# Optimization experiments

Hardware: AMD Instinct MI355X
Metric: run time of the kernel (lower is better)

## Reference

```python
import jax, jax.numpy as jnp
import numpy as np

N, Q, D = 8, 900, 256
HB, WB = 200, 200
L, NH, P = 6, 8, 4
HD = D // NH
FF = 512
NCLS, NBOX = 10, 8
ODIM = NCLS + NBOX
THRESH = 0.5
OFFSET_SCALE = 1.0
SCALE = 1.0 / float(np.sqrt(HD))


def _ln(x, g, b, eps=1e-5):
    m = jnp.mean(x, axis=-1, keepdims=True)
    v = jnp.mean((x - m) ** 2, axis=-1, keepdims=True)
    return (x - m) * jax.lax.rsqrt(v + eps) * g + b


def _mha(x, Wq, bq, Wk, bk, Wv, bv, Wo, bo):
    q = (x @ Wq + bq).reshape(N, Q, NH, HD)
    k = (x @ Wk + bk).reshape(N, Q, NH, HD)
    v = (x @ Wv + bv).reshape(N, Q, NH, HD)
    att = jax.nn.softmax(jnp.einsum('bqhd,bkhd->bhqk', q, k) * SCALE, axis=-1)
    o = jnp.einsum('bhqk,bkhd->bqhd', att, v).reshape(N, Q, D)
    return o @ Wo + bo


def _deform(q, ref, bev, dv_W, dv_b, off_W, off_b, aw_W, aw_b, do_W, do_b):
    # value projection of BEV map: (N, HW, D) -> (N, NH, HW, HD)
    val = (bev @ dv_W + dv_b).reshape(N, HB * WB, NH, HD).transpose(0, 2, 1, 3)
    off = (q @ off_W + off_b).reshape(N, Q, NH, P, 2)
    aw = jax.nn.softmax((q @ aw_W + aw_b).reshape(N, Q, NH, P), axis=-1)
    # ref: (N,Q,1,2) pixel coords -> broadcast to (N,Q,NH,P,2)
    loc = ref[:, :, :, None, :] + off * OFFSET_SCALE
    x = jnp.clip(loc[..., 0], 0.0, WB - 1.0)
    y = jnp.clip(loc[..., 1], 0.0, HB - 1.0)
    x0 = jnp.floor(x)
    y0 = jnp.floor(y)
    x1 = jnp.minimum(x0 + 1.0, WB - 1.0)
    y1 = jnp.minimum(y0 + 1.0, HB - 1.0)
    wx = (x - x0).transpose(0, 2, 1, 3)[..., None]  # (N,NH,Q,P,1)
    wy = (y - y0).transpose(0, 2, 1, 3)[..., None]

    def gather(ix, iy):
        idx = (iy * WB + ix).astype(jnp.int32)               # (N,Q,NH,P)
        idx = idx.transpose(0, 2, 1, 3).reshape(N, NH, Q * P, 1)
        g = jnp.take_along_axis(val, idx, axis=2)            # (N,NH,Q*P,HD)
        return g.reshape(N, NH, Q, P, HD)

    samp = (gather(x0, y0) * (1 - wx) * (1 - wy)
            + gather(x1, y0) * wx * (1 - wy)
            + gather(x0, y1) * (1 - wx) * wy
            + gather(x1, y1) * wx * wy)                      # (N,NH,Q,P,HD)
    awt = aw.transpose(0, 2, 1, 3)                           # (N,NH,Q,P)
    out = jnp.einsum('bhqp,bhqpd->bqhd', awt, samp).reshape(N, Q, D)
    return out @ do_W + do_b


def _ref_points():
    # n_sample=Q points evenly spread over the HBxWB grid, pixel coords, unnormalized
    idx = jnp.round(jnp.linspace(0.0, HB * WB - 1.0, Q)).astype(jnp.int32)
    x = (idx % WB).astype(jnp.float32)
    y = (idx // WB).astype(jnp.float32)
    rp = jnp.stack([x, y], axis=-1)                          # (Q,2)
    return jnp.broadcast_to(rp[None, :, None, :], (N, Q, 1, 2))


def _det(x, W1, b1, W2, b2):
    h = jax.nn.relu(x @ W1 + b1)
    o = h @ W2 + b2
    return jnp.concatenate([jax.nn.sigmoid(o[..., :NCLS]), o[..., NCLS:]], axis=-1)


def setup_inputs() -> dict:
    key = jax.random.key(0)
    ks = iter(jax.random.split(key, 48))

    def w(shape, s=0.02):
        return jax.random.normal(next(ks), shape, jnp.float32) * s

    inp = {
        'bev_features': jax.random.normal(next(ks), (N, HB * WB, D), jnp.float32),
        'pos_emb': w((Q, D), 1.0),
        'Wq': w((L, D, D)), 'bq': jnp.zeros((L, D), jnp.float32),
        'Wk': w((L, D, D)), 'bk': jnp.zeros((L, D), jnp.float32),
        'Wv': w((L, D, D)), 'bv': jnp.zeros((L, D), jnp.float32),
        'Wo': w((L, D, D)), 'bo': jnp.zeros((L, D), jnp.float32),
        'ln1_g': jnp.ones((L, D), jnp.float32), 'ln1_b': jnp.zeros((L, D), jnp.float32),
        'ln2_g': jnp.ones((L, D), jnp.float32), 'ln2_b': jnp.zeros((L, D), jnp.float32),
        'ln3_g': jnp.ones((L, D), jnp.float32), 'ln3_b': jnp.zeros((L, D), jnp.float32),
        'dv_W': w((L, D, D)), 'dv_b': jnp.zeros((L, D), jnp.float32),
        'off_W': w((L, D, NH * P * 2), 0.01), 'off_b': jnp.zeros((L, NH * P * 2), jnp.float32),
        'aw_W': w((L, D, NH * P), 0.01), 'aw_b': jnp.zeros((L, NH * P), jnp.float32),
        'do_W': w((L, D, D)), 'do_b': jnp.zeros((L, D), jnp.float32),
        'f1_W': w((L, D, FF)), 'f1_b': jnp.zeros((L, FF), jnp.float32),
        'f2_W': w((L, FF, D)), 'f2_b': jnp.zeros((L, D), jnp.float32),
        'det_W1': w((D, D)), 'det_b1': jnp.zeros((D,), jnp.float32),
        'det_W2': w((D, ODIM)), 'det_b2': jnp.zeros((ODIM,), jnp.float32),
    }
    return inp


def reference(bev_features, pos_emb, Wq, bq, Wk, bk, Wv, bv, Wo, bo,
              ln1_g, ln1_b, ln2_g, ln2_b, ln3_g, ln3_b,
              dv_W, dv_b, off_W, off_b, aw_W, aw_b, do_W, do_b,
              f1_W, f1_b, f2_W, f2_b, det_W1, det_b1, det_W2, det_b2):
    queries = jnp.broadcast_to(pos_emb[None], (N, Q, D))
    ref = _ref_points()
    output = queries
    layer_results = []
    for i in range(L):
        x = output + queries
        a = _mha(x, Wq[i], bq[i], Wk[i], bk[i], Wv[i], bv[i], Wo[i], bo[i])
        x2 = _ln(x + a, ln1_g[i], ln1_b[i])
        d = _deform(x2, ref, bev_features, dv_W[i], dv_b[i], off_W[i], off_b[i],
                    aw_W[i], aw_b[i], do_W[i], do_b[i])
        x3 = _ln(x2 + d, ln2_g[i], ln2_b[i])
        f = jax.nn.relu(x3 @ f1_W[i] + f1_b[i]) @ f2_W[i] + f2_b[i]
        output = _ln(x3 + f, ln3_g[i], ln3_b[i])
        layer_results.append(_det(output, det_W1, det_b1, det_W2, det_b2))
    layer_results = jnp.stack(layer_results, axis=0)   # (L,N,Q,ODIM)
    detections = layer_results[-1]
    track_mask = detections[..., 0] >= THRESH
    return output, detections, track_mask, layer_results
```

## Files before the change

### kernel.cpp

```cpp
#include <hip/hip_runtime.h>
#include <hip/hip_bf16.h>
#include <math.h>

#define N 8
#define Q 900
#define D 256
#define HB 200
#define WB 200
#define L 6
#define NH 8
#define P 4
#define HD 32
#define FF 512
#define NCLS 10
#define ODIM 18
#define HW (HB*WB)
#define NQ (N*Q)
#define NQD (NQ*D)
#define QD (Q*D)
#define SCALE 0.17677669529663687f

typedef __attribute__((ext_vector_type(4))) float f32x4;
typedef __attribute__((ext_vector_type(8))) short short8v;

__device__ __forceinline__ short bf16_of(float f) {
  __hip_bfloat16 h = __float2bfloat16(f);
  return __builtin_bit_cast(short, h);
}

#define TM 64
#define TN 64
#define KC 128

template <int ACT>
__global__ __launch_bounds__(256) void gemm_kernel(
    const float* __restrict__ A, const float* __restrict__ B,
    const float* __restrict__ bias, float* __restrict__ C,
    int M, int K, int Nc) {
  __shared__ float AsT[KC][TM + 4];
  __shared__ float Bs[KC][TN + 4];
  const int tid = threadIdx.x;
  const int tx = tid & 15, ty = tid >> 4;
  const int m0 = blockIdx.x * TM, n0 = blockIdx.y * TN;

  float c[4][4] = {};

  for (int kc = 0; kc < K; kc += KC) {
    {
      int r = tid >> 2;
      int gr = m0 + r;
      int kb = (tid & 3) * 32;
#pragma unroll
      for (int q = 0; q < 8; ++q) {
        int k = kb + q * 4;
        float4 av = make_float4(0.f, 0.f, 0.f, 0.f);
        if (gr < M) av = *(const float4*)(A + (size_t)gr * K + kc + k);
        AsT[k + 0][r] = av.x; AsT[k + 1][r] = av.y;
        AsT[k + 2][r] = av.z; AsT[k + 3][r] = av.w;
      }
    }
    {
#pragma unroll
      for (int i = 0; i < 8; ++i) {
        int idx = i * 256 + tid;
        int kr = idx >> 4;
        int c4 = (idx & 15) * 4;
        *(float4*)&Bs[kr][c4] = *(const float4*)(B + (size_t)(kc + kr) * Nc + n0 + c4);
      }
    }
    __syncthreads();
#pragma unroll 8
    for (int kk = 0; kk < KC; ++kk) {
      float4 av = *(const float4*)&AsT[kk][ty * 4];
      float4 bv = *(const float4*)&Bs[kk][tx * 4];
      c[0][0] += av.x * bv.x; c[0][1] += av.x * bv.y; c[0][2] += av.x * bv.z; c[0][3] += av.x * bv.w;
      c[1][0] += av.y * bv.x; c[1][1] += av.y * bv.y; c[1][2] += av.y * bv.z; c[1][3] += av.y * bv.w;
      c[2][0] += av.z * bv.x; c[2][1] += av.z * bv.y; c[2][2] += av.z * bv.z; c[2][3] += av.z * bv.w;
      c[3][0] += av.w * bv.x; c[3][1] += av.w * bv.y; c[3][2] += av.w * bv.z; c[3][3] += av.w * bv.w;
    }
    __syncthreads();
  }

#pragma unroll
  for (int i = 0; i < 4; ++i) {
    int row = m0 + ty * 4 + i;
    if (row >= M) continue;
#pragma unroll
    for (int j = 0; j < 4; ++j) {
      int col = n0 + tx * 4 + j;
      float v = c[i][j] + bias[col];
      if (ACT == 1) v = fmaxf(v, 0.f);
      C[(size_t)row * Nc + col] = v;
    }
  }
}

#define TMT 64
#define TKT 16
template <int ACT>
__global__ __launch_bounds__(256) void gemm_thin_kernel(
    const float* __restrict__ A, const float* __restrict__ B,
    const float* __restrict__ bias, float* __restrict__ C,
    int M, int K, int Nc) {
  __shared__ float AsT[TKT][TMT + 4];
  __shared__ float Bs[TKT][16 + 2];
  const int tid = threadIdx.x;
  const int tx = tid & 15, ty = tid >> 4;
  const int m0 = blockIdx.x * TMT, n0 = blockIdx.y * 16;

  float c[4] = {};

  for (int kt = 0; kt < K; kt += TKT) {
    {
      int r = tid >> 2;
      int cb = (tid & 3) * 4;
      int gr = m0 + r;
      float4 av = make_float4(0.f, 0.f, 0.f, 0.f);
      if (gr < M) av = *(const float4*)(A + (size_t)gr * K + kt + cb);
      AsT[cb + 0][r] = av.x;
      AsT[cb + 1][r] = av.y;
      AsT[cb + 2][r] = av.z;
      AsT[cb + 3][r] = av.w;
    }
    {
      int r = tid >> 4;
      int cc = tid & 15;
      int gc = n0 + cc;
      Bs[r][cc] = (gc < Nc) ? B[(size_t)(kt + r) * Nc + gc] : 0.f;
    }
    __syncthreads();
#pragma unroll
    for (int kk = 0; kk < TKT; ++kk) {
      float4 av = *(const float4*)&AsT[kk][ty * 4];
      float bv = Bs[kk][tx];
      c[0] += av.x * bv; c[1] += av.y * bv; c[2] += av.z * bv; c[3] += av.w * bv;
    }
    __syncthreads();
  }

  int col = n0 + tx;
  if (col < Nc) {
    float bs = bias[col];
#pragma unroll
    for (int i = 0; i < 4; ++i) {
      int row = m0 + ty * 4 + i;
      if (row < M) {
        float v = c[i] + bs;
        if (ACT == 2 && col < NCLS) v = 1.f / (1.f + expf(-v));
        C[(size_t)row * Nc + col] = v;
      }
    }
  }
}

__global__ __launch_bounds__(256) void attn_kernel(
    const float* __restrict__ qg, const float* __restrict__ kg,
    const float* __restrict__ vg, float* __restrict__ og) {
  const int n = blockIdx.z, h = blockIdx.y;
  const int wv = threadIdx.x >> 6;
  const int lane = threadIdx.x & 63;
  const int g = lane >> 4;
  const int c = lane & 15;
  const int q0 = blockIdx.x * 64 + wv * 16;

  const float* qb = qg + (size_t)n * Q * D + h * HD;
  const float* kb = kg + (size_t)n * Q * D + h * HD;
  const float* vb = vg + (size_t)n * Q * D + h * HD;

  short8v qf = {};
  {
    int qr = q0 + c;
    if (qr < Q) {
      const float* qp = qb + (size_t)qr * D + g * 8;
#pragma unroll
      for (int j = 0; j < 8; ++j) qf[j] = bf16_of(qp[j]);
    }
  }

  const float SC2 = SCALE * 1.4426950408889634f;
  float m2 = -1e30f, l = 0.f;
  f32x4 acc0 = {0.f, 0.f, 0.f, 0.f}, acc1 = {0.f, 0.f, 0.f, 0.f};

  for (int kt0 = 0; kt0 < Q; kt0 += 64) {
    float s[16];
#pragma unroll
    for (int t = 0; t < 4; ++t) {
      short8v kf = {};
      int kr = kt0 + t * 16 + c;
      if (kr < Q) {
        const float* kp = kb + (size_t)kr * D + g * 8;
#pragma unroll
        for (int j = 0; j < 8; ++j) kf[j] = bf16_of(kp[j]);
      }
      f32x4 d = __builtin_amdgcn_mfma_f32_16x16x32_bf16(kf, qf, (f32x4){0.f, 0.f, 0.f, 0.f}, 0, 0, 0);
#pragma unroll
      for (int r = 0; r < 4; ++r) s[t * 4 + r] = d[r];
    }
#pragma unroll
    for (int t = 0; t < 4; ++t)
#pragma unroll
      for (int r = 0; r < 4; ++r) {
        int key = kt0 + t * 16 + g * 4 + r;
        s[t * 4 + r] = (key < Q) ? s[t * 4 + r] * SC2 : -1e30f;
      }
    float tm = s[0];
#pragma unroll
    for (int j = 1; j < 16; ++j) tm = fmaxf(tm, s[j]);
    tm = fmaxf(tm, __shfl_xor(tm, 16));
    tm = fmaxf(tm, __shfl_xor(tm, 32));
    float m2n = fmaxf(m2, tm);
    float corr = exp2f(m2 - m2n);
    m2 = m2n;
    float ps = 0.f;
#pragma unroll
    for (int j = 0; j < 16; ++j) { s[j] = exp2f(s[j] - m2); ps += s[j]; }
    ps += __shfl_xor(ps, 16);
    ps += __shfl_xor(ps, 32);
    l = l * corr + ps;
    float cr0 = __shfl(corr, g * 4 + 0);
    float cr1 = __shfl(corr, g * 4 + 1);
    float cr2 = __shfl(corr, g * 4 + 2);
    float cr3 = __shfl(corr, g * 4 + 3);
    acc0[0] *= cr0; acc0[1] *= cr1; acc0[2] *= cr2; acc0[3] *= cr3;
    acc1[0] *= cr0; acc1[1] *= cr1; acc1[2] *= cr2; acc1[3] *= cr3;

#pragma unroll
    for (int pr = 0; pr < 2; ++pr) {
      short8v pa, v0 = {}, v1 = {};
#pragma unroll
      for (int j = 0; j < 8; ++j) pa[j] = bf16_of(s[pr * 8 + j]);
#pragma unroll
      for (int j = 0; j < 8; ++j) {
        int key = kt0 + (pr * 2 + (j >> 2)) * 16 + g * 4 + (j & 3);
        if (key < Q) {
          const float* vp = vb + (size_t)key * D;
          v0[j] = bf16_of(vp[c]);
          v1[j] = bf16_of(vp[c + 16]);
        }
      }
      acc0 = __builtin_amdgcn_mfma_f32_16x16x32_bf16(pa, v0, acc0, 0, 0, 0);
      acc1 = __builtin_amdgcn_mfma_f32_16x16x32_bf16(pa, v1, acc1, 0, 0, 0);
    }
  }

  float inv = 1.f / l;
  float iv[4];
#pragma unroll
  for (int r = 0; r < 4; ++r) iv[r] = __shfl(inv, g * 4 + r);
#pragma unroll
  for (int r = 0; r < 4; ++r) {
    int qr = q0 + g * 4 + r;
    if (qr < Q) {
      float* op = og + (size_t)(n * Q + qr) * D + h * HD;
      op[c] = acc0[r] * iv[r];
      op[c + 16] = acc1[r] * iv[r];
    }
  }
}

__global__ __launch_bounds__(256) void ln_add_kernel(
    const float* __restrict__ A, const float* __restrict__ Bp,
    const float* __restrict__ g, const float* __restrict__ b,
    float* __restrict__ out) {
  const int wave = threadIdx.x >> 6;
  const int lane = threadIdx.x & 63;
  const int row = blockIdx.x * 4 + wave;
  const size_t base = (size_t)row * D + lane * 4;
  float4 a4 = *(const float4*)(A + base);
  float4 b4 = *(const float4*)(Bp + base);
  float v0 = a4.x + b4.x, v1 = a4.y + b4.y, v2 = a4.z + b4.z, v3 = a4.w + b4.w;
  float sum = v0 + v1 + v2 + v3;
#pragma unroll
  for (int off = 1; off < 64; off <<= 1) sum += __shfl_xor(sum, off);
  float mean = sum * (1.f / D);
  float d0 = v0 - mean, d1 = v1 - mean, d2 = v2 - mean, d3 = v3 - mean;
  float vsum = d0 * d0 + d1 * d1 + d2 * d2 + d3 * d3;
#pragma unroll
  for (int off = 1; off < 64; off <<= 1) vsum += __shfl_xor(vsum, off);
  float inv_std = 1.0f / sqrtf(vsum * (1.f / D) + 1e-5f);
  float4 g4 = *(const float4*)(g + lane * 4);
  float4 bb4 = *(const float4*)(b + lane * 4);
  float4 o4;
  o4.x = d0 * inv_std * g4.x + bb4.x;
  o4.y = d1 * inv_std * g4.y + bb4.y;
  o4.z = d2 * inv_std * g4.z + bb4.z;
  o4.w = d3 * inv_std * g4.w + bb4.w;
  *(float4*)(out + base) = o4;
}

__global__ __launch_bounds__(256) void deform_kernel(
    const float* __restrict__ bev, const float* __restrict__ offB,
    const float* __restrict__ awB, const float* __restrict__ dvW,
    const float* __restrict__ dvb, float* __restrict__ dtmp) {
  const int pb = blockIdx.x;
  const int bq0 = pb * 2;
  const int n = bq0 / Q;
  const int t = threadIdx.x;

  __shared__ float aw_s[2][NH * P];
  __shared__ int   idx_s[2][NH * P * 4];
  __shared__ float w_s[2][NH * P * 4];
  __shared__ float agg_s[2][NH][D + 4];
  __shared__ float red_s[2][4][D];

  if (t < 64) {
    int qq = t >> 5, e = t & 31;
    int bq = bq0 + qq;
    int qi = bq - n * Q;
    float tq = __fmul_rn((float)qi, 44.492767333984375f);
    int ir = (int)rintf(tq);
    float rx = (float)(ir % WB);
    float ry = (float)(ir / WB);
    float ox = offB[(size_t)bq * 64 + e * 2 + 0];
    float oy = offB[(size_t)bq * 64 + e * 2 + 1];
    float lx = fminf(fmaxf(rx + ox, 0.f), (float)(WB - 1));
    float ly = fminf(fmaxf(ry + oy, 0.f), (float)(HB - 1));
    float x0 = floorf(lx), y0 = floorf(ly);
    float x1 = fminf(x0 + 1.f, (float)(WB - 1));
    float y1 = fminf(y0 + 1.f, (float)(HB - 1));
    float wx = lx - x0, wy = ly - y0;
    int b4 = e * 4;
    idx_s[qq][b4 + 0] = (int)y0 * WB + (int)x0; w_s[qq][b4 + 0] = (1.f - wx) * (1.f - wy);
    idx_s[qq][b4 + 1] = (int)y0 * WB + (int)x1; w_s[qq][b4 + 1] = wx * (1.f - wy);
    idx_s[qq][b4 + 2] = (int)y1 * WB + (int)x0; w_s[qq][b4 + 2] = (1.f - wx) * wy;
    idx_s[qq][b4 + 3] = (int)y1 * WB + (int)x1; w_s[qq][b4 + 3] = wx * wy;
  } else if (t < 80) {
    int qq = (t - 64) >> 3, hh = (t - 64) & 7;
    const float* ap = awB + (size_t)(bq0 + qq) * 32 + hh * P;
    float l0 = ap[0], l1 = ap[1], l2 = ap[2], l3 = ap[3];
    float mx = fmaxf(fmaxf(l0, l1), fmaxf(l2, l3));
    float e0 = expf(l0 - mx), e1 = expf(l1 - mx), e2 = expf(l2 - mx), e3 = expf(l3 - mx);
    float inv = 1.f / (e0 + e1 + e2 + e3);
    aw_s[qq][hh * P + 0] = e0 * inv; aw_s[qq][hh * P + 1] = e1 * inv;
    aw_s[qq][hh * P + 2] = e2 * inv; aw_s[qq][hh * P + 3] = e3 * inv;
  }
  __syncthreads();

  {
    const float* bevn = bev + (size_t)n * HW * D;
    const int wv = t >> 6, lane = t & 63;
    const int c4 = lane * 4;
#pragma unroll
    for (int u = 0; u < 4; ++u) {
      int pid = wv + u * 4;
      int qq = pid >> 3, h = pid & 7;
      f32x4 acc = {0.f, 0.f, 0.f, 0.f};
#pragma unroll
      for (int p = 0; p < P; ++p) {
        int e = h * P + p;
        float aw = aw_s[qq][e];
        const int* ix = &idx_s[qq][e * 4];
        const float* wsp = &w_s[qq][e * 4];
        float4 g0 = *(const float4*)(bevn + (size_t)ix[0] * D + c4);
        float4 g1 = *(const float4*)(bevn + (size_t)ix[1] * D + c4);
        float4 g2 = *(const float4*)(bevn + (size_t)ix[2] * D + c4);
        float4 g3 = *(const float4*)(bevn + (size_t)ix[3] * D + c4);
        acc[0] += aw * (wsp[0] * g0.x + wsp[1] * g1.x + wsp[2] * g2.x + wsp[3] * g3.x);
        acc[1] += aw * (wsp[0] * g0.y + wsp[1] * g1.y + wsp[2] * g2.y + wsp[3] * g3.y);
        acc[2] += aw * (wsp[0] * g0.z + wsp[1] * g1.z + wsp[2] * g2.z + wsp[3] * g3.z);
        acc[3] += aw * (wsp[0] * g0.w + wsp[1] * g1.w + wsp[2] * g2.w + wsp[3] * g3.w);
      }
      *(f32x4*)&agg_s[qq][h][c4] = acc;
    }
  }
  __syncthreads();

  {
    const int chunk = t >> 6;
    const int col4 = t & 63;
    const int tt0 = col4 * 4;
    const int h = tt0 >> 5;
    f32x4 p0 = {0.f, 0.f, 0.f, 0.f}, p1 = {0.f, 0.f, 0.f, 0.f};
    const float* ag0 = agg_s[0][h];
    const float* ag1 = agg_s[1][h];
#pragma unroll 4
    for (int dd4 = 0; dd4 < 64; dd4 += 4) {
      int dd = chunk * 64 + dd4;
      float4 w0 = *(const float4*)(dvW + (size_t)(dd + 0) * D + tt0);
      float4 w1 = *(const float4*)(dvW + (size_t)(dd + 1) * D + tt0);
      float4 w2 = *(const float4*)(dvW + (size_t)(dd + 2) * D + tt0);
      float4 w3 = *(const float4*)(dvW + (size_t)(dd + 3) * D + tt0);
      float4 a0 = *(const float4*)&ag0[dd];
      float4 a1 = *(const float4*)&ag1[dd];
      p0[0] += a0.x * w0.x + a0.y * w1.x + a0.z * w2.x + a0.w * w3.x;
      p0[1] += a0.x * w0.y + a0.y * w1.y + a0.z * w2.y + a0.w * w3.y;
      p0[2] += a0.x * w0.z + a0.y * w1.z + a0.z * w2.z + a0.w * w3.z;
      p0[3] += a0.x * w0.w + a0.y * w1.w + a0.z * w2.w + a0.w * w3.w;
      p1[0] += a1.x * w0.x + a1.y * w1.x + a1.z * w2.x + a1.w * w3.x;
      p1[1] += a1.x * w0.y + a1.y * w1.y + a1.z * w2.y + a1.w * w3.y;
      p1[2] += a1.x * w0.z + a1.y * w1.z + a1.z * w2.z + a1.w * w3.z;
      p1[3] += a1.x * w0.w + a1.y * w1.w + a1.z * w2.w + a1.w * w3.w;
    }
    *(f32x4*)&red_s[0][chunk][tt0] = p0;
    *(f32x4*)&red_s[1][chunk][tt0] = p1;
  }
  __syncthreads();
  {
    float bs = dvb[t];
    dtmp[(size_t)bq0 * D + t] =
        bs + red_s[0][0][t] + red_s[0][1][t] + red_s[0][2][t] + red_s[0][3][t];
    dtmp[(size_t)(bq0 + 1) * D + t] =
        bs + red_s[1][0][t] + red_s[1][1][t] + red_s[1][2][t] + red_s[1][3][t];
  }
}

__global__ void bcast_q_kernel(const float* __restrict__ pos, float* __restrict__ out) {
  for (size_t i = (size_t)blockIdx.x * blockDim.x + threadIdx.x; i < (size_t)NQD;
       i += (size_t)gridDim.x * blockDim.x)
    out[i] = pos[i % QD];
}
__global__ void add_q_kernel(const float* __restrict__ prev, const float* __restrict__ pos,
                             float* __restrict__ x) {
  for (size_t i = (size_t)blockIdx.x * blockDim.x + threadIdx.x; i < (size_t)NQD;
       i += (size_t)gridDim.x * blockDim.x)
    x[i] = prev[i] + pos[i % QD];
}
__global__ void finalize_kernel(const float* __restrict__ lr5, float* __restrict__ det,
                                float* __restrict__ mask) {
  int i = blockIdx.x * blockDim.x + threadIdx.x;
  if (i < NQ * ODIM) det[i] = lr5[i];
  if (i < NQ) mask[i] = (lr5[(size_t)i * ODIM] >= 0.5f) ? 1.0f : 0.0f;
}

extern "C" void kernel_launch(void* const* d_in, const int* in_sizes, int n_in,
                              void* d_out, int out_size, void* d_ws, size_t ws_size,
                              hipStream_t stream) {
  const float* bev  = (const float*)d_in[0];
  const float* pos  = (const float*)d_in[1];
  const float* Wq   = (const float*)d_in[2];  const float* bq  = (const float*)d_in[3];
  const float* Wk   = (const float*)d_in[4];  const float* bk  = (const float*)d_in[5];
  const float* Wv   = (const float*)d_in[6];  const float* bv  = (const float*)d_in[7];
  const float* Wo   = (const float*)d_in[8];  const float* bo  = (const float*)d_in[9];
  const float* ln1g = (const float*)d_in[10]; const float* ln1b = (const float*)d_in[11];
  const float* ln2g = (const float*)d_in[12]; const float* ln2b = (const float*)d_in[13];
  const float* ln3g = (const float*)d_in[14]; const float* ln3b = (const float*)d_in[15];
  const float* dvW  = (const float*)d_in[16]; const float* dvb = (const float*)d_in[17];
  const float* offW = (const float*)d_in[18]; const float* offb = (const float*)d_in[19];
  const float* awW  = (const float*)d_in[20]; const float* awb = (const float*)d_in[21];
  const float* doW  = (const float*)d_in[22]; const float* dob = (const float*)d_in[23];
  const float* f1W  = (const float*)d_in[24]; const float* f1b = (const float*)d_in[25];
  const float* f2W  = (const float*)d_in[26]; const float* f2b = (const float*)d_in[27];
  const float* dW1  = (const float*)d_in[28]; const float* db1 = (const float*)d_in[29];
  const float* dW2  = (const float*)d_in[30]; const float* db2 = (const float*)d_in[31];

  float* w = (float*)d_ws;
  float* b0 = w + 0 * (size_t)NQD;
  float* b1 = w + 1 * (size_t)NQD;
  float* b2 = w + 2 * (size_t)NQD;
  float* b3 = w + 3 * (size_t)NQD;
  float* ffh = b1;
  float* offB = b0;
  float* awB  = b0 + (size_t)NQ * 64;

  float* out_output = (float*)d_out;
  float* out_det    = out_output + (size_t)NQD;
  float* out_mask   = out_det + (size_t)NQ * ODIM;
  float* out_lr     = out_mask + (size_t)NQ;

  const dim3 blk256(256);
  const dim3 gemmGridD((NQ + TM - 1) / TM, D / TN);
  const dim3 gemmGridFF((NQ + TM - 1) / TM, FF / TN);
  const dim3 thinGridOff((NQ + TMT - 1) / TMT, 4);
  const dim3 thinGridAw((NQ + TMT - 1) / TMT, 2);
  const dim3 thinGridDet((NQ + TMT - 1) / TMT, 2);
  const dim3 attnGrid((Q + 63) / 64, NH, N);
  const dim3 lnGrid(NQ / 4);
  const dim3 defGrid(NQ / 2);
  const int ewGrid = 1024;

  bcast_q_kernel<<<ewGrid, blk256, 0, stream>>>(pos, out_output);

  for (int i = 0; i < L; ++i) {
    const size_t wDD = (size_t)i * D * D;
    add_q_kernel<<<ewGrid, blk256, 0, stream>>>(out_output, pos, b0);
    gemm_kernel<0><<<gemmGridD, blk256, 0, stream>>>(b0, Wq + wDD, bq + (size_t)i * D, b1, NQ, D, D);
    gemm_kernel<0><<<gemmGridD, blk256, 0, stream>>>(b0, Wk + wDD, bk + (size_t)i * D, b2, NQ, D, D);
    gemm_kernel<0><<<gemmGridD, blk256, 0, stream>>>(b0, Wv + wDD, bv + (size_t)i * D, b3, NQ, D, D);
    attn_kernel<<<attnGrid, blk256, 0, stream>>>(b1, b2, b3, out_output);
    gemm_kernel<0><<<gemmGridD, blk256, 0, stream>>>(out_output, Wo + wDD, bo + (size_t)i * D, b1, NQ, D, D);
    ln_add_kernel<<<lnGrid, blk256, 0, stream>>>(b0, b1, ln1g + (size_t)i * D, ln1b + (size_t)i * D, b2);
    gemm_thin_kernel<0><<<thinGridOff, blk256, 0, stream>>>(b2, offW + (size_t)i * D * 64, offb + (size_t)i * 64, offB, NQ, D, 64);
    gemm_thin_kernel<0><<<thinGridAw, blk256, 0, stream>>>(b2, awW + (size_t)i * D * 32, awb + (size_t)i * 32, awB, NQ, D, 32);
    deform_kernel<<<defGrid, blk256, 0, stream>>>(bev, offB, awB, dvW + wDD, dvb + (size_t)i * D, b3);
    gemm_kernel<0><<<gemmGridD, blk256, 0, stream>>>(b3, doW + wDD, dob + (size_t)i * D, b1, NQ, D, D);
    ln_add_kernel<<<lnGrid, blk256, 0, stream>>>(b2, b1, ln2g + (size_t)i * D, ln2b + (size_t)i * D, b0);
    gemm_kernel<1><<<gemmGridFF, blk256, 0, stream>>>(b0, f1W + (size_t)i * D * FF, f1b + (size_t)i * FF, ffh, NQ, D, FF);
    gemm_kernel<0><<<gemmGridD, blk256, 0, stream>>>(ffh, f2W + (size_t)i * FF * D, f2b + (size_t)i * D, b3, NQ, FF, D);
    ln_add_kernel<<<lnGrid, blk256, 0, stream>>>(b0, b3, ln3g + (size_t)i * D, ln3b + (size_t)i * D, out_output);
    gemm_kernel<1><<<gemmGridD, blk256, 0, stream>>>(out_output, dW1, db1, b1, NQ, D, D);
    gemm_thin_kernel<2><<<thinGridDet, blk256, 0, stream>>>(b1, dW2, db2, out_lr + (size_t)i * NQ * ODIM, NQ, D, ODIM);
  }

  finalize_kernel<<<(NQ * ODIM + 255) / 256, blk256, 0, stream>>>(out_lr + (size_t)(L - 1) * NQ * ODIM,
                                                                  out_det, out_mask);
}
```

Measured before the change: 2.639 ms.

## Fuse QKV projections, off/aw projections, pos-add into LN, and widen deform blocks

Merges the three Q/K/V GEMM launches into one grid that selects the weight matrix by blockIdx.y, and folds the pos-embedding add into that GEMM's A-tile load and into a new three-input LayerNorm kernel. The separate add_q pass and its buffer round trip go away. The offset and attention-weight thin GEMMs become one launch. The deform kernel now handles four queries per block instead of two, so each dvW tile load is reused across more queries, at the cost of more shared memory per block and fewer blocks.

```diff
diff --git a/kernel.cpp b/kernel.cpp
--- a/kernel.cpp
+++ b/kernel.cpp
@@ -95,6 +95,79 @@
   }
 }
 
+__global__ __launch_bounds__(256) void gemm_qkv_kernel(
+    const float* __restrict__ outp, const float* __restrict__ pos,
+    const float* __restrict__ Wq, const float* __restrict__ bq,
+    const float* __restrict__ Wk, const float* __restrict__ bk,
+    const float* __restrict__ Wv, const float* __restrict__ bv,
+    float* __restrict__ Oq, float* __restrict__ Ok, float* __restrict__ Ov) {
+  __shared__ float AsT[KC][TM + 4];
+  __shared__ float Bs[KC][TN + 4];
+  const int tid = threadIdx.x;
+  const int tx = tid & 15, ty = tid >> 4;
+  const int m0 = blockIdx.x * TM;
+  const int wsel = blockIdx.y >> 2;
+  const int n0 = (blockIdx.y & 3) * TN;
+  const float* B = (wsel == 0) ? Wq : (wsel == 1) ? Wk : Wv;
+  const float* bias = (wsel == 0) ? bq : (wsel == 1) ? bk : bv;
+  float* C = (wsel == 0) ? Oq : (wsel == 1) ? Ok : Ov;
+
+  float c[4][4] = {};
+
+  for (int kc = 0; kc < D; kc += KC) {
+    {
+      int r = tid >> 2;
+      int gr = m0 + r;
+      int kb = (tid & 3) * 32;
+      const float* ar = outp + (size_t)gr * D + kc;
+      const float* pr = pos + (size_t)(gr % Q) * D + kc;
+#pragma unroll
+      for (int q = 0; q < 8; ++q) {
+        int k = kb + q * 4;
+        float4 av = make_float4(0.f, 0.f, 0.f, 0.f);
+        if (gr < NQ) {
+          float4 ov = *(const float4*)(ar + k);
+          float4 pv = *(const float4*)(pr + k);
+          av.x = ov.x + pv.x; av.y = ov.y + pv.y; av.z = ov.z + pv.z; av.w = ov.w + pv.w;
+        }
+        AsT[k + 0][r] = av.x; AsT[k + 1][r] = av.y;
+        AsT[k + 2][r] = av.z; AsT[k + 3][r] = av.w;
+      }
+    }
+    {
+#pragma unroll
+      for (int i = 0; i < 8; ++i) {
+        int idx = i * 256 + tid;
+        int kr = idx >> 4;
+        int c4 = (idx & 15) * 4;
+        *(float4*)&Bs[kr][c4] = *(const float4*)(B + (size_t)(kc + kr) * D + n0 + c4);
+      }
+    }
+    __syncthreads();
+#pragma unroll 8
+    for (int kk = 0; kk < KC; ++kk) {
+      float4 av = *(const float4*)&AsT[kk][ty * 4];
+      float4 bv4 = *(const float4*)&Bs[kk][tx * 4];
+      c[0][0] += av.x * bv4.x; c[0][1] += av.x * bv4.y; c[0][2] += av.x * bv4.z; c[0][3] += av.x * bv4.w;
+      c[1][0] += av.y * bv4.x; c[1][1] += av.y * bv4.y; c[1][2] += av.y * bv4.z; c[1][3] += av.y * bv4.w;
+      c[2][0] += av.z * bv4.x; c[2][1] += av.z * bv4.y; c[2][2] += av.z * bv4.z; c[2][3] += av.z * bv4.w;
+      c[3][0] += av.w * bv4.x; c[3][1] += av.w * bv4.y; c[3][2] += av.w * bv4.z; c[3][3] += av.w * bv4.w;
+    }
+    __syncthreads();
+  }
+
+#pragma unroll
+  for (int i = 0; i < 4; ++i) {
+    int row = m0 + ty * 4 + i;
+    if (row >= NQ) continue;
+#pragma unroll
+    for (int j = 0; j < 4; ++j) {
+      int col = n0 + tx * 4 + j;
+      C[(size_t)row * D + col] = c[i][j] + bias[col];
+    }
+  }
+}
+
 #define TMT 64
 #define TKT 16
 template <int ACT>
@@ -153,6 +226,61 @@
   }
 }
 
+__global__ __launch_bounds__(256) void gemm_offaw_kernel(
+    const float* __restrict__ A,
+    const float* __restrict__ offW, const float* __restrict__ offb,
+    const float* __restrict__ awW, const float* __restrict__ awb,
+    float* __restrict__ offC, float* __restrict__ awC) {
+  __shared__ float AsT[TKT][TMT + 4];
+  __shared__ float Bs[TKT][16 + 2];
+  const int tid = threadIdx.x;
+  const int tx = tid & 15, ty = tid >> 4;
+  const int m0 = blockIdx.x * TMT;
+  const bool isOff = blockIdx.y < 4;
+  const int n0 = isOff ? blockIdx.y * 16 : (blockIdx.y - 4) * 16;
+  const int Nc = isOff ? 64 : 32;
+  const float* B = isOff ? offW : awW;
+  const float* bias = isOff ? offb : awb;
+  float* C = isOff ? offC : awC;
+
+  float c[4] = {};
+
+  for (int kt = 0; kt < D; kt += TKT) {
+    {
+      int r = tid >> 2;
+      int cb = (tid & 3) * 4;
+      int gr = m0 + r;
+      float4 av = make_float4(0.f, 0.f, 0.f, 0.f);
+      if (gr < NQ) av = *(const float4*)(A + (size_t)gr * D + kt + cb);
+      AsT[cb + 0][r] = av.x;
+      AsT[cb + 1][r] = av.y;
+      AsT[cb + 2][r] = av.z;
+      AsT[cb + 3][r] = av.w;
+    }
+    {
+      int r = tid >> 4;
+      int cc = tid & 15;
+      Bs[r][cc] = B[(size_t)(kt + r) * Nc + n0 + cc];
+    }
+    __syncthreads();
+#pragma unroll
+    for (int kk = 0; kk < TKT; ++kk) {
+      float4 av = *(const float4*)&AsT[kk][ty * 4];
+      float bv = Bs[kk][tx];
+      c[0] += av.x * bv; c[1] += av.y * bv; c[2] += av.z * bv; c[3] += av.w * bv;
+    }
+    __syncthreads();
+  }
+
+  int col = n0 + tx;
+  float bs = bias[col];
+#pragma unroll
+  for (int i = 0; i < 4; ++i) {
+    int row = m0 + ty * 4 + i;
+    if (row < NQ) C[(size_t)row * Nc + col] = c[i] + bs;
+  }
+}
+
 __global__ __launch_bounds__(256) void attn_kernel(
     const float* __restrict__ qg, const float* __restrict__ kg,
     const float* __restrict__ vg, float* __restrict__ og) {
@@ -288,22 +416,55 @@
   *(float4*)(out + base) = o4;
 }
 
+__global__ __launch_bounds__(256) void ln_add3_kernel(
+    const float* __restrict__ A, const float* __restrict__ pos,
+    const float* __restrict__ Bp,
+    const float* __restrict__ g, const float* __restrict__ b,
+    float* __restrict__ out) {
+  const int wave = threadIdx.x >> 6;
+  const int lane = threadIdx.x & 63;
+  const int row = blockIdx.x * 4 + wave;
+  const size_t base = (size_t)row * D + lane * 4;
+  const size_t pbase = (size_t)(row % Q) * D + lane * 4;
+  float4 a4 = *(const float4*)(A + base);
+  float4 p4 = *(const float4*)(pos + pbase);
+  float4 b4 = *(const float4*)(Bp + base);
+  float x0 = a4.x + p4.x, x1 = a4.y + p4.y, x2 = a4.z + p4.z, x3 = a4.w + p4.w;
+  float v0 = x0 + b4.x, v1 = x1 + b4.y, v2 = x2 + b4.z, v3 = x3 + b4.w;
+  float sum = v0 + v1 + v2 + v3;
+#pragma unroll
+  for (int off = 1; off < 64; off <<= 1) sum += __shfl_xor(sum, off);
+  float mean = sum * (1.f / D);
+  float d0 = v0 - mean, d1 = v1 - mean, d2 = v2 - mean, d3 = v3 - mean;
+  float vsum = d0 * d0 + d1 * d1 + d2 * d2 + d3 * d3;
+#pragma unroll
+  for (int off = 1; off < 64; off <<= 1) vsum += __shfl_xor(vsum, off);
+  float inv_std = 1.0f / sqrtf(vsum * (1.f / D) + 1e-5f);
+  float4 g4 = *(const float4*)(g + lane * 4);
+  float4 bb4 = *(const float4*)(b + lane * 4);
+  float4 o4;
+  o4.x = d0 * inv_std * g4.x + bb4.x;
+  o4.y = d1 * inv_std * g4.y + bb4.y;
+  o4.z = d2 * inv_std * g4.z + bb4.z;
+  o4.w = d3 * inv_std * g4.w + bb4.w;
+  *(float4*)(out + base) = o4;
+}
+
 __global__ __launch_bounds__(256) void deform_kernel(
     const float* __restrict__ bev, const float* __restrict__ offB,
     const float* __restrict__ awB, const float* __restrict__ dvW,
     const float* __restrict__ dvb, float* __restrict__ dtmp) {
-  const int pb = blockIdx.x;
-  const int bq0 = pb * 2;
+  const int bq0 = blockIdx.x * 4;
   const int n = bq0 / Q;
   const int t = threadIdx.x;
 
-  __shared__ float aw_s[2][NH * P];
-  __shared__ int   idx_s[2][NH * P * 4];
-  __shared__ float w_s[2][NH * P * 4];
-  __shared__ float agg_s[2][NH][D + 4];
-  __shared__ float red_s[2][4][D];
-
-  if (t < 64) {
+  __shared__ float aw_s[4][NH * P];
+  __shared__ int   idx_s[4][NH * P * 4];
+  __shared__ float w_s[4][NH * P * 4];
+  __shared__ float agg_s[4][NH][D];
+  __shared__ float red_s[4][4][D];
+
+  if (t < 128) {
     int qq = t >> 5, e = t & 31;
     int bq = bq0 + qq;
     int qi = bq - n * Q;
@@ -324,8 +485,9 @@
     idx_s[qq][b4 + 1] = (int)y0 * WB + (int)x1; w_s[qq][b4 + 1] = wx * (1.f - wy);
     idx_s[qq][b4 + 2] = (int)y1 * WB + (int)x0; w_s[qq][b4 + 2] = (1.f - wx) * wy;
     idx_s[qq][b4 + 3] = (int)y1 * WB + (int)x1; w_s[qq][b4 + 3] = wx * wy;
-  } else if (t < 80) {
-    int qq = (t - 64) >> 3, hh = (t - 64) & 7;
+  } else if (t < 160) {
+    int idx = t - 128;
+    int qq = idx >> 3, hh = idx & 7;
     const float* ap = awB + (size_t)(bq0 + qq) * 32 + hh * P;
     float l0 = ap[0], l1 = ap[1], l2 = ap[2], l3 = ap[3];
     float mx = fmaxf(fmaxf(l0, l1), fmaxf(l2, l3));
@@ -341,7 +503,7 @@
     const int wv = t >> 6, lane = t & 63;
     const int c4 = lane * 4;
 #pragma unroll
-    for (int u = 0; u < 4; ++u) {
+    for (int u = 0; u < 8; ++u) {
       int pid = wv + u * 4;
       int qq = pid >> 3, h = pid & 7;
       f32x4 acc = {0.f, 0.f, 0.f, 0.f};
@@ -370,9 +532,7 @@
     const int col4 = t & 63;
     const int tt0 = col4 * 4;
     const int h = tt0 >> 5;
-    f32x4 p0 = {0.f, 0.f, 0.f, 0.f}, p1 = {0.f, 0.f, 0.f, 0.f};
-    const float* ag0 = agg_s[0][h];
-    const float* ag1 = agg_s[1][h];
+    f32x4 p[4] = {{0.f,0.f,0.f,0.f},{0.f,0.f,0.f,0.f},{0.f,0.f,0.f,0.f},{0.f,0.f,0.f,0.f}};
 #pragma unroll 4
     for (int dd4 = 0; dd4 < 64; dd4 += 4) {
       int dd = chunk * 64 + dd4;
@@ -380,27 +540,26 @@
       float4 w1 = *(const float4*)(dvW + (size_t)(dd + 1) * D + tt0);
       float4 w2 = *(const float4*)(dvW + (size_t)(dd + 2) * D + tt0);
       float4 w3 = *(const float4*)(dvW + (size_t)(dd + 3) * D + tt0);
-      float4 a0 = *(const float4*)&ag0[dd];
-      float4 a1 = *(const float4*)&ag1[dd];
-      p0[0] += a0.x * w0.x + a0.y * w1.x + a0.z * w2.x + a0.w * w3.x;
-      p0[1] += a0.x * w0.y + a0.y * w1.y + a0.z * w2.y + a0.w * w3.y;
-      p0[2] += a0.x * w0.z + a0.y * w1.z + a0.z * w2.z + a0.w * w3.z;
-      p0[3] += a0.x * w0.w + a0.y * w1.w + a0.z * w2.w + a0.w * w3.w;
-      p1[0] += a1.x * w0.x + a1.y * w1.x + a1.z * w2.x + a1.w * w3.x;
-      p1[1] += a1.x * w0.y + a1.y * w1.y + a1.z * w2.y + a1.w * w3.y;
-      p1[2] += a1.x * w0.z + a1.y * w1.z + a1.z * w2.z + a1.w * w3.z;
-      p1[3] += a1.x * w0.w + a1.y * w1.w + a1.z * w2.w + a1.w * w3.w;
-    }
-    *(f32x4*)&red_s[0][chunk][tt0] = p0;
-    *(f32x4*)&red_s[1][chunk][tt0] = p1;
+#pragma unroll
+      for (int qq = 0; qq < 4; ++qq) {
+        float4 a = *(const float4*)&agg_s[qq][h][dd];
+        p[qq][0] += a.x * w0.x + a.y * w1.x + a.z * w2.x + a.w * w3.x;
+        p[qq][1] += a.x * w0.y + a.y * w1.y + a.z * w2.y + a.w * w3.y;
+        p[qq][2] += a.x * w0.z + a.y * w1.z + a.z * w2.z + a.w * w3.z;
+        p[qq][3] += a.x * w0.w + a.y * w1.w + a.z * w2.w + a.w * w3.w;
+      }
+    }
+#pragma unroll
+    for (int qq = 0; qq < 4; ++qq) *(f32x4*)&red_s[qq][chunk][tt0] = p[qq];
   }
   __syncthreads();
   {
     float bs = dvb[t];
-    dtmp[(size_t)bq0 * D + t] =
-        bs + red_s[0][0][t] + red_s[0][1][t] + red_s[0][2][t] + red_s[0][3][t];
-    dtmp[(size_t)(bq0 + 1) * D + t] =
-        bs + red_s[1][0][t] + red_s[1][1][t] + red_s[1][2][t] + red_s[1][3][t];
+#pragma unroll
+    for (int qq = 0; qq < 4; ++qq) {
+      dtmp[(size_t)(bq0 + qq) * D + t] =
+          bs + red_s[qq][0][t] + red_s[qq][1][t] + red_s[qq][2][t] + red_s[qq][3][t];
+    }
   }
 }
 
@@ -408,12 +567,6 @@
   for (size_t i = (size_t)blockIdx.x * blockDim.x + threadIdx.x; i < (size_t)NQD;
        i += (size_t)gridDim.x * blockDim.x)
     out[i] = pos[i % QD];
-}
-__global__ void add_q_kernel(const float* __restrict__ prev, const float* __restrict__ pos,
-                             float* __restrict__ x) {
-  for (size_t i = (size_t)blockIdx.x * blockDim.x + threadIdx.x; i < (size_t)NQD;
-       i += (size_t)gridDim.x * blockDim.x)
-    x[i] = prev[i] + pos[i % QD];
 }
 __global__ void finalize_kernel(const float* __restrict__ lr5, float* __restrict__ det,
                                 float* __restrict__ mask) {
@@ -458,29 +611,30 @@
   float* out_lr     = out_mask + (size_t)NQ;
 
   const dim3 blk256(256);
+  const dim3 qkvGrid((NQ + TM - 1) / TM, 12);
   const dim3 gemmGridD((NQ + TM - 1) / TM, D / TN);
   const dim3 gemmGridFF((NQ + TM - 1) / TM, FF / TN);
-  const dim3 thinGridOff((NQ + TMT - 1) / TMT, 4);
-  const dim3 thinGridAw((NQ + TMT - 1) / TMT, 2);
+  const dim3 offawGrid((NQ + TMT - 1) / TMT, 6);
   const dim3 thinGridDet((NQ + TMT - 1) / TMT, 2);
   const dim3 attnGrid((Q + 63) / 64, NH, N);
   const dim3 lnGrid(NQ / 4);
-  const dim3 defGrid(NQ / 2);
+  const dim3 defGrid(NQ / 4);
   const int ewGrid = 1024;
 
   bcast_q_kernel<<<ewGrid, blk256, 0, stream>>>(pos, out_output);
 
   for (int i = 0; i < L; ++i) {
     const size_t wDD = (size_t)i * D * D;
-    add_q_kernel<<<ewGrid, blk256, 0, stream>>>(out_output, pos, b0);
-    gemm_kernel<0><<<gemmGridD, blk256, 0, stream>>>(b0, Wq + wDD, bq + (size_t)i * D, b1, NQ, D, D);
-    gemm_kernel<0><<<gemmGridD, blk256, 0, stream>>>(b0, Wk + wDD, bk + (size_t)i * D, b2, NQ, D, D);
-    gemm_kernel<0><<<gemmGridD, blk256, 0, stream>>>(b0, Wv + wDD, bv + (size_t)i * D, b3, NQ, D, D);
-    attn_kernel<<<attnGrid, blk256, 0, stream>>>(b1, b2, b3, out_output);
-    gemm_kernel<0><<<gemmGridD, blk256, 0, stream>>>(out_output, Wo + wDD, bo + (size_t)i * D, b1, NQ, D, D);
-    ln_add_kernel<<<lnGrid, blk256, 0, stream>>>(b0, b1, ln1g + (size_t)i * D, ln1b + (size_t)i * D, b2);
-    gemm_thin_kernel<0><<<thinGridOff, blk256, 0, stream>>>(b2, offW + (size_t)i * D * 64, offb + (size_t)i * 64, offB, NQ, D, 64);
-    gemm_thin_kernel<0><<<thinGridAw, blk256, 0, stream>>>(b2, awW + (size_t)i * D * 32, awb + (size_t)i * 32, awB, NQ, D, 32);
+    gemm_qkv_kernel<<<qkvGrid, blk256, 0, stream>>>(out_output, pos,
+        Wq + wDD, bq + (size_t)i * D, Wk + wDD, bk + (size_t)i * D,
+        Wv + wDD, bv + (size_t)i * D, b1, b2, b3);
+    attn_kernel<<<attnGrid, blk256, 0, stream>>>(b1, b2, b3, b0);
+    gemm_kernel<0><<<gemmGridD, blk256, 0, stream>>>(b0, Wo + wDD, bo + (size_t)i * D, b1, NQ, D, D);
+    ln_add3_kernel<<<lnGrid, blk256, 0, stream>>>(out_output, pos, b1,
+        ln1g + (size_t)i * D, ln1b + (size_t)i * D, b2);
+    gemm_offaw_kernel<<<offawGrid, blk256, 0, stream>>>(b2,
+        offW + (size_t)i * D * 64, offb + (size_t)i * 64,
+        awW + (size_t)i * D * 32, awb + (size_t)i * 32, offB, awB);
     deform_kernel<<<defGrid, blk256, 0, stream>>>(bev, offB, awB, dvW + wDD, dvb + (size_t)i * D, b3);
     gemm_kernel<0><<<gemmGridD, blk256, 0, stream>>>(b3, doW + wDD, dob + (size_t)i * D, b1, NQ, D, D);
     ln_add_kernel<<<lnGrid, blk256, 0, stream>>>(b2, b1, ln2g + (size_t)i * D, ln2b + (size_t)i * D, b0);
```

Result: faster. 2.522 ms (-4.4%).
